# Kernel tuning notes

Hardware: AMD Instinct MI355X
Metric: run time of the kernel (lower is better)

## Reference

```python
import jax, jax.numpy as jnp
import numpy as np

ALIGNED_H = 7
ALIGNED_W = 7
IMG_H, IMG_W = 800.0, 1216.0


def setup_inputs() -> dict:
    key = jax.random.key(0)
    k1, k2, k3, k4 = jax.random.split(key, 4)
    N, C, H, W = 2, 256, 200, 304
    R = 2000
    features = jax.random.normal(k1, (N, C, H, W), dtype=jnp.float32)
    # rois: [batch_idx, x1, y1, x2, y2] in image coordinates
    bidx = jax.random.randint(k2, (R,), 0, N).astype(jnp.float32)
    xy1 = jax.random.uniform(k3, (R, 2)) * jnp.array([IMG_W * 0.7, IMG_H * 0.7])
    wh = 16.0 + jax.random.uniform(k4, (R, 2)) * jnp.array([IMG_W * 0.3 - 16.0, IMG_H * 0.3 - 16.0])
    xy2 = jnp.minimum(xy1 + wh, jnp.array([IMG_W - 1.0, IMG_H - 1.0]))
    rois = jnp.concatenate([bidx[:, None], xy1[:, 0:1], xy1[:, 1:2], xy2[:, 0:1], xy2[:, 1:2]], axis=1).astype(jnp.float32)
    spatial_scale = jnp.float32(0.25)
    return {"features": features, "rois": rois, "spatial_scale": spatial_scale}


def roi_align(features, rois, spatial_scale, ah, aw):
    N, C, H, W = features.shape
    b = rois[:, 0].astype(jnp.int32)                       # [R]
    x1 = rois[:, 1] * spatial_scale
    y1 = rois[:, 2] * spatial_scale
    x2 = rois[:, 3] * spatial_scale
    y2 = rois[:, 4] * spatial_scale
    roi_w = jnp.maximum(x2 - x1 + 1.0, 0.0)
    roi_h = jnp.maximum(y2 - y1 + 1.0, 0.0)
    bin_h = roi_h / (ah - 1.0)                             # [R]
    bin_w = roi_w / (aw - 1.0)
    ph = jnp.arange(ah, dtype=jnp.float32)
    pw = jnp.arange(aw, dtype=jnp.float32)
    h = y1[:, None] + ph[None, :] * bin_h[:, None]         # [R, ah]
    w = x1[:, None] + pw[None, :] * bin_w[:, None]         # [R, aw]
    valid = ((h >= 0) & (h < H))[:, :, None] & ((w >= 0) & (w < W))[:, None, :]  # [R, ah, aw]
    hs = jnp.clip(jnp.floor(h), 0.0, H - 2.0)              # kernel: min(floor(h), H-2)
    ws = jnp.clip(jnp.floor(w), 0.0, W - 2.0)
    dh = (h - hs)[:, :, None]                              # [R, ah, 1]
    dw = (w - ws)[:, None, :]                              # [R, 1, aw]
    yi = hs.astype(jnp.int32)[:, :, None]                  # [R, ah, 1]
    xi = ws.astype(jnp.int32)[:, None, :]                  # [R, 1, aw]
    bi = b[:, None, None]                                  # [R, 1, 1]
    # gather 4 corners -> [R, ah, aw, C]
    v00 = features[bi, :, yi, xi]
    v01 = features[bi, :, yi, xi + 1]
    v10 = features[bi, :, yi + 1, xi]
    v11 = features[bi, :, yi + 1, xi + 1]
    dh4 = dh[..., None]
    dw4 = dw[..., None]
    val = (v00 * (1 - dh4) * (1 - dw4) + v01 * (1 - dh4) * dw4
           + v10 * dh4 * (1 - dw4) + v11 * dh4 * dw4)
    out = jnp.where(valid[..., None], val, 0.0)            # [R, ah, aw, C]
    return jnp.transpose(out, (0, 3, 1, 2))                # [R, C, ah, aw]


def reference(features, rois, spatial_scale):
    return roi_align(features, rois, spatial_scale, ALIGNED_H, ALIGNED_W)
```

## Files before the change

### kernel.cpp

```cpp
#include <hip/hip_runtime.h>

#define C_ 256
#define H_ 200
#define W_ 304
#define AH 7
#define AW 7
#define KK (AH * AW)
#define SP 260

__device__ __forceinline__ unsigned short bf16_rn(float f) {
    unsigned int u = __float_as_uint(f);
    unsigned int r = (u + 0x7FFFu + ((u >> 16) & 1u)) >> 16;
    return (unsigned short)r;
}
__device__ __forceinline__ float b2f(unsigned short s) {
    return __uint_as_float((unsigned int)s << 16);
}

__global__ __launch_bounds__(256) void transpose_nchw_nhwc_bf16(
    const float* __restrict__ in, unsigned short* __restrict__ out) {
    __shared__ float tile[128][65];
    const int HW = H_ * W_;
    const int n  = blockIdx.z;
    const int p0 = blockIdx.x * 64;
    const int c0 = blockIdx.y * 128;
    const float* inb = in + (size_t)n * C_ * HW;
    unsigned short* outb = out + (size_t)n * HW * C_;

    {
        const int q  = threadIdx.x & 15;
        const int r0 = threadIdx.x >> 4;
        #pragma unroll
        for (int i = 0; i < 8; ++i) {
            const int c = r0 + 16 * i;
            const float4 v = *(const float4*)&inb[(size_t)(c0 + c) * HW + p0 + 4 * q];
            tile[c][4 * q + 0] = v.x;
            tile[c][4 * q + 1] = v.y;
            tile[c][4 * q + 2] = v.z;
            tile[c][4 * q + 3] = v.w;
        }
    }
    __syncthreads();
    {
        const int cq = threadIdx.x & 31;
        const int pr = threadIdx.x >> 5;
        #pragma unroll
        for (int i = 0; i < 8; ++i) {
            const int p = pr + 8 * i;
            ushort4 o;
            o.x = bf16_rn(tile[4 * cq + 0][p]);
            o.y = bf16_rn(tile[4 * cq + 1][p]);
            o.z = bf16_rn(tile[4 * cq + 2][p]);
            o.w = bf16_rn(tile[4 * cq + 3][p]);
            *(ushort4*)&outb[(size_t)(p0 + p) * C_ + c0 + 4 * cq] = o;
        }
    }
}

__global__ __launch_bounds__(256) void roialign_nhwc_bf16(
    const unsigned short* __restrict__ tf, const float* __restrict__ rois,
    const float* __restrict__ scale_ptr, float* __restrict__ out) {
    __shared__ float sout[KK * SP];
    const int r    = blockIdx.x;
    const int wave = threadIdx.x >> 6;
    const int lane = threadIdx.x & 63;
    const int c4   = lane * 4;

    const float scale = scale_ptr[0];
    const float* roi = rois + (size_t)r * 5;
    const int   b  = (int)roi[0];
    const float x1 = roi[1] * scale;
    const float y1 = roi[2] * scale;
    const float x2 = roi[3] * scale;
    const float y2 = roi[4] * scale;
    const float roi_w = fmaxf(x2 - x1 + 1.0f, 0.0f);
    const float roi_h = fmaxf(y2 - y1 + 1.0f, 0.0f);
    const float bin_h = roi_h / (float)(AH - 1);
    const float bin_w = roi_w / (float)(AW - 1);
    const unsigned short* fb = tf + (size_t)b * (H_ * W_) * C_;

    for (int k = wave; k < KK; k += 4) {
        const int ph = k / AW;
        const int pw = k - ph * AW;
        const float h  = y1 + (float)ph * bin_h;
        const float w  = x1 + (float)pw * bin_w;
        const float hs = fminf(fmaxf(floorf(h), 0.0f), (float)(H_ - 2));
        const float ws = fminf(fmaxf(floorf(w), 0.0f), (float)(W_ - 2));
        const float dh = h - hs;
        const float dw = w - ws;
        const int   yi = (int)hs;
        const int   xi = (int)ws;
        const bool  valid = (h >= 0.0f) && (h < (float)H_) &&
                            (w >= 0.0f) && (w < (float)W_);
        const unsigned short* p = fb + ((size_t)yi * W_ + xi) * C_ + c4;
        const ushort4 a00 = *(const ushort4*)p;
        const ushort4 a01 = *(const ushort4*)(p + C_);
        const ushort4 a10 = *(const ushort4*)(p + (size_t)W_ * C_);
        const ushort4 a11 = *(const ushort4*)(p + (size_t)W_ * C_ + C_);
        const float w00 = (1.0f - dh) * (1.0f - dw);
        const float w01 = (1.0f - dh) * dw;
        const float w10 = dh * (1.0f - dw);
        const float w11 = dh * dw;
        float4 v;
        v.x = b2f(a00.x) * w00 + b2f(a01.x) * w01 + b2f(a10.x) * w10 + b2f(a11.x) * w11;
        v.y = b2f(a00.y) * w00 + b2f(a01.y) * w01 + b2f(a10.y) * w10 + b2f(a11.y) * w11;
        v.z = b2f(a00.z) * w00 + b2f(a01.z) * w01 + b2f(a10.z) * w10 + b2f(a11.z) * w11;
        v.w = b2f(a00.w) * w00 + b2f(a01.w) * w01 + b2f(a10.w) * w10 + b2f(a11.w) * w11;
        if (!valid) { v.x = 0.0f; v.y = 0.0f; v.z = 0.0f; v.w = 0.0f; }
        *(float4*)&sout[k * SP + c4] = v;
    }
    __syncthreads();
    float* ob = out + (size_t)r * C_ * KK;
    for (int i = threadIdx.x; i < C_ * KK; i += 256) {
        const int c = i / KK;
        const int k = i - c * KK;
        ob[i] = sout[k * SP + c];
    }
}

__global__ __launch_bounds__(256) void roialign_nchw(
    const float* __restrict__ feat, const float* __restrict__ rois,
    const float* __restrict__ scale_ptr, float* __restrict__ out) {
    __shared__ float sout[C_ * KK];
    const int r = blockIdx.x;
    const int c = threadIdx.x;
    const float scale = scale_ptr[0];
    const float* roi = rois + (size_t)r * 5;
    const int   b  = (int)roi[0];
    const float x1 = roi[1] * scale;
    const float y1 = roi[2] * scale;
    const float x2 = roi[3] * scale;
    const float y2 = roi[4] * scale;
    const float roi_w = fmaxf(x2 - x1 + 1.0f, 0.0f);
    const float roi_h = fmaxf(y2 - y1 + 1.0f, 0.0f);
    const float bin_h = roi_h / (float)(AH - 1);
    const float bin_w = roi_w / (float)(AW - 1);
    const float* fb = feat + ((size_t)b * C_ + c) * (H_ * W_);

    for (int ph = 0; ph < AH; ++ph) {
        const float h  = y1 + (float)ph * bin_h;
        const float hs = fminf(fmaxf(floorf(h), 0.0f), (float)(H_ - 2));
        const float dh = h - hs;
        const int   yi = (int)hs;
        const bool  vh = (h >= 0.0f) && (h < (float)H_);
        #pragma unroll
        for (int pw = 0; pw < AW; ++pw) {
            const float w  = x1 + (float)pw * bin_w;
            const float ws = fminf(fmaxf(floorf(w), 0.0f), (float)(W_ - 2));
            const float dw = w - ws;
            const int   xi = (int)ws;
            const bool  valid = vh && (w >= 0.0f) && (w < (float)W_);
            const float v00 = fb[(size_t)yi * W_ + xi];
            const float v01 = fb[(size_t)yi * W_ + xi + 1];
            const float v10 = fb[(size_t)(yi + 1) * W_ + xi];
            const float v11 = fb[(size_t)(yi + 1) * W_ + xi + 1];
            float val = v00 * (1.0f - dh) * (1.0f - dw)
                      + v01 * (1.0f - dh) * dw
                      + v10 * dh * (1.0f - dw)
                      + v11 * dh * dw;
            sout[c * KK + ph * AW + pw] = valid ? val : 0.0f;
        }
    }
    __syncthreads();
    float* ob = out + (size_t)r * C_ * KK;
    #pragma unroll 4
    for (int i = threadIdx.x; i < C_ * KK; i += 256) ob[i] = sout[i];
}

extern "C" void kernel_launch(void* const* d_in, const int* in_sizes, int n_in,
                              void* d_out, int out_size, void* d_ws, size_t ws_size,
                              hipStream_t stream) {
    const float* feat  = (const float*)d_in[0];
    const float* rois  = (const float*)d_in[1];
    const float* scale = (const float*)d_in[2];
    float* out = (float*)d_out;

    const int R = in_sizes[1] / 5;
    const int N = in_sizes[0] / (C_ * H_ * W_);
    const size_t need = (size_t)N * C_ * H_ * W_ * sizeof(unsigned short);

    if (ws_size >= need) {
        unsigned short* tf = (unsigned short*)d_ws;
        dim3 tb(256);
        dim3 tg((H_ * W_) / 64, C_ / 128, N);
        hipLaunchKernelGGL(transpose_nchw_nhwc_bf16, tg, tb, 0, stream, feat, tf);
        hipLaunchKernelGGL(roialign_nhwc_bf16, dim3(R), dim3(256), 0, stream,
                           tf, rois, scale, out);
    } else {
        hipLaunchKernelGGL(roialign_nchw, dim3(R), dim3(256), 0, stream,
                           feat, rois, scale, out);
    }
}
```

Measured before the change: 79.00 us.

## Convert to bf16 before LDS staging, widen transpose and output stores

The transpose kernel now converts to packed bf16 when loading into shared memory. This halves the LDS tile, and each thread reads 8 channel words and shuffles them into two 16-byte NHWC stores instead of 8-byte ones. In the ROI kernel the bin loop gets a partial unroll, and the final shared-to-global copy writes float4 vectors instead of scalars. The intent is fewer LDS and global store transactions; the price is extra integer pack/shuffle work and possible LDS bank conflicts from the new tile stride.

```diff
diff --git a/kernel.cpp b/kernel.cpp
--- a/kernel.cpp
+++ b/kernel.cpp
@@ -1,4 +1,5 @@
 #include <hip/hip_runtime.h>
+#include <hip/hip_bf16.h>
 
 #define C_ 256
 #define H_ 200
@@ -8,18 +9,13 @@
 #define KK (AH * AW)
 #define SP 260
 
-__device__ __forceinline__ unsigned short bf16_rn(float f) {
-    unsigned int u = __float_as_uint(f);
-    unsigned int r = (u + 0x7FFFu + ((u >> 16) & 1u)) >> 16;
-    return (unsigned short)r;
-}
 __device__ __forceinline__ float b2f(unsigned short s) {
     return __uint_as_float((unsigned int)s << 16);
 }
 
 __global__ __launch_bounds__(256) void transpose_nchw_nhwc_bf16(
     const float* __restrict__ in, unsigned short* __restrict__ out) {
-    __shared__ float tile[128][65];
+    __shared__ unsigned int tile[128][34];
     const int HW = H_ * W_;
     const int n  = blockIdx.z;
     const int p0 = blockIdx.x * 64;
@@ -34,25 +30,34 @@
         for (int i = 0; i < 8; ++i) {
             const int c = r0 + 16 * i;
             const float4 v = *(const float4*)&inb[(size_t)(c0 + c) * HW + p0 + 4 * q];
-            tile[c][4 * q + 0] = v.x;
-            tile[c][4 * q + 1] = v.y;
-            tile[c][4 * q + 2] = v.z;
-            tile[c][4 * q + 3] = v.w;
+            const __hip_bfloat162 lo = __float22bfloat162_rn(make_float2(v.x, v.y));
+            const __hip_bfloat162 hi = __float22bfloat162_rn(make_float2(v.z, v.w));
+            unsigned int ulo, uhi;
+            __builtin_memcpy(&ulo, &lo, 4);
+            __builtin_memcpy(&uhi, &hi, 4);
+            *(uint2*)&tile[c][2 * q] = make_uint2(ulo, uhi);
         }
     }
     __syncthreads();
     {
-        const int cq = threadIdx.x & 31;
-        const int pr = threadIdx.x >> 5;
-        #pragma unroll
-        for (int i = 0; i < 8; ++i) {
-            const int p = pr + 8 * i;
-            ushort4 o;
-            o.x = bf16_rn(tile[4 * cq + 0][p]);
-            o.y = bf16_rn(tile[4 * cq + 1][p]);
-            o.z = bf16_rn(tile[4 * cq + 2][p]);
-            o.w = bf16_rn(tile[4 * cq + 3][p]);
-            *(ushort4*)&outb[(size_t)(p0 + p) * C_ + c0 + 4 * cq] = o;
+        const int pp0 = threadIdx.x & 15;
+        const int cq  = threadIdx.x >> 4;
+        #pragma unroll
+        for (int i = 0; i < 2; ++i) {
+            const int pp = pp0 + 16 * i;
+            unsigned int u[8];
+            #pragma unroll
+            for (int j = 0; j < 8; ++j) u[j] = tile[8 * cq + j][pp];
+            unsigned int pe[4], po[4];
+            #pragma unroll
+            for (int k = 0; k < 4; ++k) {
+                pe[k] = (u[2 * k] & 0xFFFFu) | (u[2 * k + 1] << 16);
+                po[k] = (u[2 * k] >> 16) | (u[2 * k + 1] & 0xFFFF0000u);
+            }
+            unsigned short* oA = &outb[(size_t)(p0 + 2 * pp) * C_ + c0 + 8 * cq];
+            unsigned short* oB = oA + C_;
+            *(uint4*)oA = make_uint4(pe[0], pe[1], pe[2], pe[3]);
+            *(uint4*)oB = make_uint4(po[0], po[1], po[2], po[3]);
         }
     }
 }
@@ -79,6 +84,7 @@
     const float bin_w = roi_w / (float)(AW - 1);
     const unsigned short* fb = tf + (size_t)b * (H_ * W_) * C_;
 
+    #pragma unroll 2
     for (int k = wave; k < KK; k += 4) {
         const int ph = k / AW;
         const int pw = k - ph * AW;
@@ -111,10 +117,18 @@
     }
     __syncthreads();
     float* ob = out + (size_t)r * C_ * KK;
-    for (int i = threadIdx.x; i < C_ * KK; i += 256) {
-        const int c = i / KK;
-        const int k = i - c * KK;
-        ob[i] = sout[k * SP + c];
+    const int nf4 = C_ * KK / 4;
+    for (int idx = threadIdx.x; idx < nf4; idx += 256) {
+        const int f = 4 * idx;
+        float4 v;
+        #pragma unroll
+        for (int e = 0; e < 4; ++e) {
+            const int fe = f + e;
+            const int c = fe / KK;
+            const int k = fe - c * KK;
+            (&v.x)[e] = sout[k * SP + c];
+        }
+        *(float4*)&ob[f] = v;
     }
 }
 
```

After: 80.80 us. +2.3%, slower.
